# Kernel tuning notes

Hardware: AMD Instinct MI355X
Metric: run time of the kernel (lower is better)

Reference implementation:

```python
import jax, jax.numpy as jnp
import numpy as np

ALPHA = 1.0
BETA = 1.0
INPUT_DIM = 64
OUTPUT_DIM = 128
DEGREE = 4


def setup_inputs() -> dict:
    key = jax.random.key(0)
    k1, k2 = jax.random.split(key)
    x = jax.random.normal(k1, (4, INPUT_DIM, 65536), dtype=jnp.float32)
    std = 1.0 / (INPUT_DIM * (DEGREE + 1))
    jacobi_coeffs = std * jax.random.normal(k2, (INPUT_DIM, OUTPUT_DIM, DEGREE + 1), dtype=jnp.float32)
    return {"x": x, "jacobi_coeffs": jacobi_coeffs}


def _jacobi_basis(x, degree, a, b):
    # x: (b, s, i). Returns list of degree+1 arrays of shape (b, s, i).
    polys = [jnp.ones_like(x)]
    if degree > 0:
        polys.append((a - b + (a + b + 2.0) * x) / 2.0)
    for i in range(2, degree + 1):
        A = (2 * i + a + b - 1) * (2 * i + a + b) / (2 * i * (i + a + b))
        B = (2 * i + a + b - 1) * (a ** 2 - b ** 2) / (2 * i * (i + a + b) * (2 * i + a + b - 2))
        C = -2 * (i + a - 1) * (i + b - 1) * (2 * i + a + b) / (2 * i * (i + a + b) * (2 * i + a + b - 2))
        polys.append((A * x + B) * polys[i - 1] + C * polys[i - 2])
    return polys


def reference(x, jacobi_coeffs):
    a, b, degree = ALPHA, BETA, DEGREE
    # x: (b, i, s) -> (b, s, i)
    xt = jnp.tanh(jnp.transpose(x, (0, 2, 1)))
    # jacobi: (b, s, i, d)
    jacobi = jnp.stack(_jacobi_basis(xt, degree, a, b), axis=-1)
    # contract over input_dim i and degree d -> (b, o, s)
    y = jnp.einsum('bsid,iod->bos', jacobi, jacobi_coeffs)
    return y
```

## Files before the change

### kernel.cpp

```cpp
#include <hip/hip_runtime.h>
#include <hip/hip_bf16.h>


#define II 64
#define SS 65536
#define OO 128

typedef __attribute__((ext_vector_type(8))) short short8;
typedef __attribute__((ext_vector_type(4))) float f32x4;
typedef __attribute__((ext_vector_type(16))) float f32x16;

__global__ __launch_bounds__(256)
void kan_prep_coeffs(const float* __restrict__ coeffs, ushort* __restrict__ cws) {
    int n = blockIdx.x * 256 + threadIdx.x;
    int i = n / 640;
    int rem = n - i * 640;
    int o = rem / 5;
    int d = rem - o * 5;
    if (d == 0) return;
    int kp = (d - 1) * 64 + i;
    int byte = (o * 512 + kp * 2) ^ ((o & 7) << 4);
    __hip_bfloat16 h = __float2bfloat16(coeffs[n]);
    cws[byte >> 1] = *reinterpret_cast<ushort*>(&h);
}

__global__ __launch_bounds__(128)
void kan_prep_bias(const float* __restrict__ coeffs, float* __restrict__ bias) {
    int o = threadIdx.x;
    float s = 0.f;
    #pragma unroll
    for (int i = 0; i < 64; ++i) s += coeffs[i * 640 + o * 5];
    bias[o] = s;
}

__device__ __forceinline__ float fast_tanh(float v) {
    float e = exp2f(v * 2.885390082f);
    float r = __builtin_amdgcn_rcpf(e + 1.0f);
    return fmaf(-2.0f, r, 1.0f);
}

__device__ __forceinline__ short8 pack8(const float* p) {
    union { short8 v; uint u[4]; } r;
    #pragma unroll
    for (int q = 0; q < 4; ++q) {
        __hip_bfloat162 h = __float22bfloat162_rn(make_float2(p[2*q], p[2*q+1]));
        r.u[q] = *reinterpret_cast<uint*>(&h);
    }
    return r.v;
}

__global__ __launch_bounds__(256)
void kan_mfma(const float* __restrict__ x, const ushort* __restrict__ cws,
              const float* __restrict__ bias, float* __restrict__ y) {
    __shared__ __align__(16) ushort clds[32768];

    const int tid  = threadIdx.x;
    const int w    = tid >> 6;
    const int l    = tid & 63;
    const int lh   = l >> 5;
    const int ls   = l & 31;
    const int b    = blockIdx.y;
    const int sgrp = blockIdx.x;

    const char* gsrc  = (const char*)cws;
    char*       lbase = (char*)clds;
    #pragma unroll
    for (int q = 0; q < 16; ++q) {
        int off = (q * 256 + tid) * 16;
        __builtin_amdgcn_global_load_lds(
            (const __attribute__((address_space(1))) uint*)(gsrc + off),
            (__attribute__((address_space(3))) uint*)(lbase + off),
            16, 0, 0);
    }
    __syncthreads();

    const int sbase = sgrp * 512 + w * 128;
    const float* xb = x + (size_t)b * II * SS;
    const int swz = (ls & 7) << 4;

    float xbuf[2][4][8];

    #pragma unroll
    for (int ig = 0; ig < 4; ++ig) {
        const float* xp = xb + (size_t)(ig * 16 + 8 * lh) * SS + sbase + ls;
        #pragma unroll
        for (int j = 0; j < 8; ++j) xbuf[0][ig][j] = xp[(size_t)j * SS];
    }

    #pragma unroll
    for (int st = 0; st < 4; ++st) {
        const int cur = st & 1;
        const int s0  = sbase + st * 32;

        if (st < 3) {
            #pragma unroll
            for (int ig = 0; ig < 4; ++ig) {
                const float* xp = xb + (size_t)(ig * 16 + 8 * lh) * SS + sbase + (st + 1) * 32 + ls;
                #pragma unroll
                for (int j = 0; j < 8; ++j) xbuf[cur ^ 1][ig][j] = xp[(size_t)j * SS];
            }
        }

        f32x16 acc[4];
        #pragma unroll
        for (int ot = 0; ot < 4; ++ot) {
            #pragma unroll
            for (int q = 0; q < 4; ++q) {
                f32x4 bv = *(const f32x4*)(bias + ot * 32 + q * 8 + 4 * lh);
                #pragma unroll
                for (int r = 0; r < 4; ++r) acc[ot][q * 4 + r] = bv[r];
            }
        }

        #pragma unroll
        for (int ig = 0; ig < 4; ++ig) {
            float p1a[8], p2a[8], p3a[8], p4a[8];
            #pragma unroll
            for (int j = 0; j < 8; ++j) {
                float t  = fast_tanh(xbuf[cur][ig][j]);
                float p1 = t + t;
                float p2 = fmaf(1.875f * t, p1, -0.75f);
                float p3 = fmaf(1.8666666666666667f * t, p2, -0.8f * p1);
                float p4 = fmaf(1.875f * t, p3, -0.8333333333333333f * p2);
                p1a[j] = p1; p2a[j] = p2; p3a[j] = p3; p4a[j] = p4;
            }
            short8 bf[4];
            bf[0] = pack8(p1a); bf[1] = pack8(p2a);
            bf[2] = pack8(p3a); bf[3] = pack8(p4a);

            #pragma unroll
            for (int di = 0; di < 4; ++di) {
                const int kt = di * 4 + ig;
                #pragma unroll
                for (int ot = 0; ot < 4; ++ot) {
                    const int o    = ot * 32 + ls;
                    const int boff = (o * 512 + kt * 32 + 16 * lh) ^ swz;
                    short8 a = *(const short8*)(lbase + boff);
                    acc[ot] = __builtin_amdgcn_mfma_f32_32x32x16_bf16(a, bf[di], acc[ot], 0, 0, 0);
                }
            }
        }

        #pragma unroll
        for (int ot = 0; ot < 4; ++ot) {
            #pragma unroll
            for (int q = 0; q < 4; ++q) {
                #pragma unroll
                for (int rr = 0; rr < 4; ++rr) {
                    const int orow = ot * 32 + rr + 8 * q + 4 * lh;
                    y[(size_t)(b * OO + orow) * SS + s0 + ls] = acc[ot][q * 4 + rr];
                }
            }
        }
    }
}

extern "C" void kernel_launch(void* const* d_in, const int* in_sizes, int n_in,
                              void* d_out, int out_size, void* d_ws, size_t ws_size,
                              hipStream_t stream) {
    const float* x      = (const float*)d_in[0];
    const float* coeffs = (const float*)d_in[1];
    float* y            = (float*)d_out;

    ushort* cws  = (ushort*)d_ws;
    float*  bias = (float*)((char*)d_ws + 65536);

    kan_prep_coeffs<<<dim3(160), dim3(256), 0, stream>>>(coeffs, cws);
    kan_prep_bias  <<<dim3(1),   dim3(128), 0, stream>>>(coeffs, bias);
    kan_mfma       <<<dim3(128, 4), dim3(256), 0, stream>>>(x, cws, bias, y);
}
```

Before: 202.6 us.

## Split output channels across two wave groups with 512-thread blocks

New measurement: 279.8 us. +38.1%, slower.

```diff
diff --git a/kernel.cpp b/kernel.cpp
--- a/kernel.cpp
+++ b/kernel.cpp
@@ -49,13 +49,15 @@
     return r.v;
 }
 
-__global__ __launch_bounds__(256)
+__global__ __launch_bounds__(512, 4)
 void kan_mfma(const float* __restrict__ x, const ushort* __restrict__ cws,
               const float* __restrict__ bias, float* __restrict__ y) {
     __shared__ __align__(16) ushort clds[32768];
 
     const int tid  = threadIdx.x;
     const int w    = tid >> 6;
+    const int ws   = w & 3;
+    const int wo   = w >> 2;
     const int l    = tid & 63;
     const int lh   = l >> 5;
     const int ls   = l & 31;
@@ -65,8 +67,8 @@
     const char* gsrc  = (const char*)cws;
     char*       lbase = (char*)clds;
     #pragma unroll
-    for (int q = 0; q < 16; ++q) {
-        int off = (q * 256 + tid) * 16;
+    for (int q = 0; q < 8; ++q) {
+        int off = (q * 512 + tid) * 16;
         __builtin_amdgcn_global_load_lds(
             (const __attribute__((address_space(1))) uint*)(gsrc + off),
             (__attribute__((address_space(3))) uint*)(lbase + off),
@@ -74,39 +76,28 @@
     }
     __syncthreads();
 
-    const int sbase = sgrp * 512 + w * 128;
-    const float* xb = x + (size_t)b * II * SS;
-    const int swz = (ls & 7) << 4;
-
-    float xbuf[2][4][8];
-
-    #pragma unroll
-    for (int ig = 0; ig < 4; ++ig) {
-        const float* xp = xb + (size_t)(ig * 16 + 8 * lh) * SS + sbase + ls;
-        #pragma unroll
-        for (int j = 0; j < 8; ++j) xbuf[0][ig][j] = xp[(size_t)j * SS];
-    }
+    const float* xb  = x + (size_t)b * II * SS;
+    const int    swz = (ls & 7) << 4;
+    const int    ob  = wo * 64;
 
     #pragma unroll
     for (int st = 0; st < 4; ++st) {
-        const int cur = st & 1;
-        const int s0  = sbase + st * 32;
+        const int s0 = sgrp * 512 + st * 128 + ws * 32;
 
-        if (st < 3) {
+        float xbuf[4][8];
+        #pragma unroll
+        for (int ig = 0; ig < 4; ++ig) {
+            const float* xp = xb + (size_t)(ig * 16 + 8 * lh) * SS + s0 + ls;
             #pragma unroll
-            for (int ig = 0; ig < 4; ++ig) {
-                const float* xp = xb + (size_t)(ig * 16 + 8 * lh) * SS + sbase + (st + 1) * 32 + ls;
-                #pragma unroll
-                for (int j = 0; j < 8; ++j) xbuf[cur ^ 1][ig][j] = xp[(size_t)j * SS];
-            }
+            for (int j = 0; j < 8; ++j) xbuf[ig][j] = xp[(size_t)j * SS];
         }
 
-        f32x16 acc[4];
+        f32x16 acc[2];
         #pragma unroll
-        for (int ot = 0; ot < 4; ++ot) {
+        for (int ot = 0; ot < 2; ++ot) {
             #pragma unroll
             for (int q = 0; q < 4; ++q) {
-                f32x4 bv = *(const f32x4*)(bias + ot * 32 + q * 8 + 4 * lh);
+                f32x4 bv = *(const f32x4*)(bias + ob + ot * 32 + q * 8 + 4 * lh);
                 #pragma unroll
                 for (int r = 0; r < 4; ++r) acc[ot][q * 4 + r] = bv[r];
             }
@@ -117,7 +108,7 @@
             float p1a[8], p2a[8], p3a[8], p4a[8];
             #pragma unroll
             for (int j = 0; j < 8; ++j) {
-                float t  = fast_tanh(xbuf[cur][ig][j]);
+                float t  = fast_tanh(xbuf[ig][j]);
                 float p1 = t + t;
                 float p2 = fmaf(1.875f * t, p1, -0.75f);
                 float p3 = fmaf(1.8666666666666667f * t, p2, -0.8f * p1);
@@ -132,8 +123,8 @@
             for (int di = 0; di < 4; ++di) {
                 const int kt = di * 4 + ig;
                 #pragma unroll
-                for (int ot = 0; ot < 4; ++ot) {
-                    const int o    = ot * 32 + ls;
+                for (int ot = 0; ot < 2; ++ot) {
+                    const int o    = ob + ot * 32 + ls;
                     const int boff = (o * 512 + kt * 32 + 16 * lh) ^ swz;
                     short8 a = *(const short8*)(lbase + boff);
                     acc[ot] = __builtin_amdgcn_mfma_f32_32x32x16_bf16(a, bf[di], acc[ot], 0, 0, 0);
@@ -142,12 +133,12 @@
         }
 
         #pragma unroll
-        for (int ot = 0; ot < 4; ++ot) {
+        for (int ot = 0; ot < 2; ++ot) {
             #pragma unroll
             for (int q = 0; q < 4; ++q) {
                 #pragma unroll
                 for (int rr = 0; rr < 4; ++rr) {
-                    const int orow = ot * 32 + rr + 8 * q + 4 * lh;
+                    const int orow = ob + ot * 32 + rr + 8 * q + 4 * lh;
                     y[(size_t)(b * OO + orow) * SS + s0 + ls] = acc[ot][q * 4 + rr];
                 }
             }
@@ -167,5 +158,5 @@
 
     kan_prep_coeffs<<<dim3(160), dim3(256), 0, stream>>>(coeffs, cws);
     kan_prep_bias  <<<dim3(1),   dim3(128), 0, stream>>>(coeffs, bias);
-    kan_mfma       <<<dim3(128, 4), dim3(256), 0, stream>>>(x, cws, bias, y);
+    kan_mfma       <<<dim3(128, 4), dim3(512), 0, stream>>>(x, cws, bias, y);
 }
```

## Process two interleaved sample columns per lane with float2 loads and stores

Applied to the files above, without the earlier changes.

Result: faster. 193.5 us (-4.5%).

```diff
diff --git a/kernel.cpp b/kernel.cpp
--- a/kernel.cpp
+++ b/kernel.cpp
@@ -49,6 +49,21 @@
     return r.v;
 }
 
+__device__ __forceinline__ void make_frags(const float xv[8], short8 bf[4]) {
+    float p1a[8], p2a[8], p3a[8], p4a[8];
+    #pragma unroll
+    for (int j = 0; j < 8; ++j) {
+        float t  = fast_tanh(xv[j]);
+        float p1 = t + t;
+        float p2 = fmaf(1.875f * t, p1, -0.75f);
+        float p3 = fmaf(1.8666666666666667f * t, p2, -0.8f * p1);
+        float p4 = fmaf(1.875f * t, p3, -0.8333333333333333f * p2);
+        p1a[j] = p1; p2a[j] = p2; p3a[j] = p3; p4a[j] = p4;
+    }
+    bf[0] = pack8(p1a); bf[1] = pack8(p2a);
+    bf[2] = pack8(p3a); bf[3] = pack8(p4a);
+}
+
 __global__ __launch_bounds__(256)
 void kan_mfma(const float* __restrict__ x, const ushort* __restrict__ cws,
               const float* __restrict__ bias, float* __restrict__ y) {
@@ -74,59 +89,53 @@
     }
     __syncthreads();
 
-    const int sbase = sgrp * 512 + w * 128;
-    const float* xb = x + (size_t)b * II * SS;
-    const int swz = (ls & 7) << 4;
-
-    float xbuf[2][4][8];
+    const float* xb    = x + (size_t)b * II * SS;
+    const int    swz   = (ls & 7) << 4;
+    const int    wbase = sgrp * 512 + w * 128;
 
     #pragma unroll
-    for (int ig = 0; ig < 4; ++ig) {
-        const float* xp = xb + (size_t)(ig * 16 + 8 * lh) * SS + sbase + ls;
-        #pragma unroll
-        for (int j = 0; j < 8; ++j) xbuf[0][ig][j] = xp[(size_t)j * SS];
-    }
+    for (int stp = 0; stp < 2; ++stp) {
+        const int s0 = wbase + stp * 64;
 
-    #pragma unroll
-    for (int st = 0; st < 4; ++st) {
-        const int cur = st & 1;
-        const int s0  = sbase + st * 32;
-
-        if (st < 3) {
-            #pragma unroll
-            for (int ig = 0; ig < 4; ++ig) {
-                const float* xp = xb + (size_t)(ig * 16 + 8 * lh) * SS + sbase + (st + 1) * 32 + ls;
-                #pragma unroll
-                for (int j = 0; j < 8; ++j) xbuf[cur ^ 1][ig][j] = xp[(size_t)j * SS];
-            }
-        }
-
-        f32x16 acc[4];
+        f32x16 accA[4], accB[4];
         #pragma unroll
         for (int ot = 0; ot < 4; ++ot) {
             #pragma unroll
             for (int q = 0; q < 4; ++q) {
                 f32x4 bv = *(const f32x4*)(bias + ot * 32 + q * 8 + 4 * lh);
                 #pragma unroll
-                for (int r = 0; r < 4; ++r) acc[ot][q * 4 + r] = bv[r];
+                for (int r = 0; r < 4; ++r) {
+                    accA[ot][q * 4 + r] = bv[r];
+                    accB[ot][q * 4 + r] = bv[r];
+                }
             }
+        }
+
+        float2 xv[2][8];
+        #pragma unroll
+        for (int j = 0; j < 8; ++j) {
+            const float2* xp = (const float2*)(xb + (size_t)(8 * lh + j) * SS + s0);
+            xv[0][j] = xp[ls];
         }
 
         #pragma unroll
         for (int ig = 0; ig < 4; ++ig) {
-            float p1a[8], p2a[8], p3a[8], p4a[8];
+            const int cur = ig & 1;
+            if (ig < 3) {
+                #pragma unroll
+                for (int j = 0; j < 8; ++j) {
+                    const float2* xp = (const float2*)(xb + (size_t)((ig + 1) * 16 + 8 * lh + j) * SS + s0);
+                    xv[cur ^ 1][j] = xp[ls];
+                }
+            }
+
+            float xa[8], xo[8];
             #pragma unroll
-            for (int j = 0; j < 8; ++j) {
-                float t  = fast_tanh(xbuf[cur][ig][j]);
-                float p1 = t + t;
-                float p2 = fmaf(1.875f * t, p1, -0.75f);
-                float p3 = fmaf(1.8666666666666667f * t, p2, -0.8f * p1);
-                float p4 = fmaf(1.875f * t, p3, -0.8333333333333333f * p2);
-                p1a[j] = p1; p2a[j] = p2; p3a[j] = p3; p4a[j] = p4;
-            }
-            short8 bf[4];
-            bf[0] = pack8(p1a); bf[1] = pack8(p2a);
-            bf[2] = pack8(p3a); bf[3] = pack8(p4a);
+            for (int j = 0; j < 8; ++j) { xa[j] = xv[cur][j].x; xo[j] = xv[cur][j].y; }
+
+            short8 bfA[4], bfB[4];
+            make_frags(xa, bfA);
+            make_frags(xo, bfB);
 
             #pragma unroll
             for (int di = 0; di < 4; ++di) {
@@ -136,7 +145,8 @@
                     const int o    = ot * 32 + ls;
                     const int boff = (o * 512 + kt * 32 + 16 * lh) ^ swz;
                     short8 a = *(const short8*)(lbase + boff);
-                    acc[ot] = __builtin_amdgcn_mfma_f32_32x32x16_bf16(a, bf[di], acc[ot], 0, 0, 0);
+                    accA[ot] = __builtin_amdgcn_mfma_f32_32x32x16_bf16(a, bfA[di], accA[ot], 0, 0, 0);
+                    accB[ot] = __builtin_amdgcn_mfma_f32_32x32x16_bf16(a, bfB[di], accB[ot], 0, 0, 0);
                 }
             }
         }
@@ -147,8 +157,12 @@
             for (int q = 0; q < 4; ++q) {
                 #pragma unroll
                 for (int rr = 0; rr < 4; ++rr) {
+                    const int reg  = q * 4 + rr;
                     const int orow = ot * 32 + rr + 8 * q + 4 * lh;
-                    y[(size_t)(b * OO + orow) * SS + s0 + ls] = acc[ot][q * 4 + rr];
+                    float2 v;
+                    v.x = accA[ot][reg];
+                    v.y = accB[ot][reg];
+                    *(float2*)(y + (size_t)(b * OO + orow) * SS + s0 + 2 * ls) = v;
                 }
             }
         }
```
